# Performance work log

Measured on AMD Instinct MI355X. Metric: run time of the kernel, lower is better.

Reference implementation:

```python
import jax, jax.numpy as jnp
import numpy as np

N_NODES = 100000
IN_CH = 256
HIDDEN = 256
N_EDGES = 500000


def setup_inputs() -> dict:
    key = jax.random.key(0)
    k_emb, k_ei, k_w1, k_w2 = jax.random.split(key, 4)
    embeddings = jax.random.normal(k_emb, (N_NODES, IN_CH), dtype=jnp.float32)
    edge_index = jax.random.randint(k_ei, (2, N_EDGES), 0, N_NODES, dtype=jnp.int64)
    # Linear(in*2, hidden) and Linear(hidden, 1) weights (stored input-major for x @ W)
    s1 = 1.0 / np.sqrt(2 * IN_CH)
    s2 = 1.0 / np.sqrt(HIDDEN)
    W1 = jax.random.uniform(k_w1, (2 * IN_CH, HIDDEN), dtype=jnp.float32, minval=-s1, maxval=s1)
    b1 = jnp.zeros((HIDDEN,), dtype=jnp.float32)
    W2 = jax.random.uniform(k_w2, (HIDDEN, 1), dtype=jnp.float32, minval=-s2, maxval=s2)
    b2 = jnp.zeros((1,), dtype=jnp.float32)
    return {"embeddings": embeddings, "edge_index": edge_index,
            "W1": W1, "b1": b1, "W2": W2, "b2": b2}


def reference(embeddings, edge_index, W1, b1, W2, b2):
    src, dst = edge_index[0], edge_index[1]
    # gather [E, in] twice, concat -> [E, 2*in]
    feats = jnp.concatenate([embeddings[src], embeddings[dst]], axis=-1)
    h = jax.nn.relu(feats @ W1 + b1)          # [E, hidden]
    scores = h @ W2 + b2                      # [E, 1]
    return scores.reshape(-1)
```

## Files before the change

kernel.cpp:

```cpp
#include <hip/hip_runtime.h>

#define NN   100000
#define EE   500000
#define MPAD 100096

using bf16x8 = __attribute__((ext_vector_type(8))) short;
using f32x4  = __attribute__((ext_vector_type(4))) float;
using u16x8  = __attribute__((ext_vector_type(8))) unsigned short;

__device__ __forceinline__ unsigned short f2bf(float f) {
  unsigned int x = __builtin_bit_cast(unsigned int, f);
  x += 0x7fffu + ((x >> 16) & 1u);
  return (unsigned short)(x >> 16);
}
__device__ __forceinline__ float bf2f(unsigned short u) {
  unsigned int x = ((unsigned int)u) << 16;
  return __builtin_bit_cast(float, x);
}

__global__ void wprep_kernel(const float* __restrict__ W1, unsigned short* __restrict__ WT) {
  int id = blockIdx.x * blockDim.x + threadIdx.x;
  if (id >= 512 * 32) return;
  int j  = id >> 5;
  int cg = id & 31;
  int jc = j & 255;
  int kb = (cg << 3) + ((j >= 256) ? 256 : 0);
  u16x8 v;
#pragma unroll
  for (int t = 0; t < 8; ++t)
    v[t] = f2bf(W1[(size_t)(kb + t) * 256 + jc]);
  *reinterpret_cast<u16x8*>(WT + (size_t)j * 256 + (cg << 3)) = v;
}

__global__ __launch_bounds__(512) void gemm_pq(const float* __restrict__ emb,
                                               const unsigned short* __restrict__ WT,
                                               unsigned short* __restrict__ R) {
  __shared__ unsigned short ldsA[2][128 * 32];
  __shared__ unsigned short ldsB[2][256 * 32];

  const int t    = threadIdx.x;
  const int lane = t & 63;
  const int wave = t >> 6;
  const int wrow = wave >> 2;
  const int wcol = wave & 3;
  const int m0   = (int)(blockIdx.x >> 1) * 128;
  const int n0   = (int)(blockIdx.x & 1) * 256;

  const int arow = t >> 2, ac = t & 3;
  const bool aOk = (m0 + arow) < NN;
  const float* aSrc = emb + (size_t)(m0 + arow) * 256 + (ac << 3);
  const int aW = arow * 32 + ((ac ^ ((arow >> 1) & 3)) << 3);

  const int brow = t >> 1, bh = t & 1;
  const unsigned short* bSrc = WT + (size_t)(n0 + brow) * 256 + (bh << 4);
  const int f_b = (brow >> 1) & 3;
  const int bW0 = brow * 32 + ((((bh << 1) | 0) ^ f_b) << 3);
  const int bW1 = brow * 32 + ((((bh << 1) | 1) ^ f_b) << 3);

  const int fr = lane & 15, fq = lane >> 4;
  int aoff[4], boff[4];
#pragma unroll
  for (int m = 0; m < 4; ++m) {
    int r = wrow * 64 + 16 * m + fr;
    aoff[m] = r * 32 + ((fq ^ ((r >> 1) & 3)) << 3);
  }
#pragma unroll
  for (int n = 0; n < 4; ++n) {
    int r = wcol * 64 + 16 * n + fr;
    boff[n] = r * 32 + ((fq ^ ((r >> 1) & 3)) << 3);
  }

  f32x4 acc[4][4] = {};

  {
    float4 a0, a1;
    if (aOk) { a0 = *(const float4*)aSrc; a1 = *(const float4*)(aSrc + 4); }
    else     { a0 = make_float4(0.f, 0.f, 0.f, 0.f); a1 = a0; }
    u16x8 b0 = *(const u16x8*)bSrc;
    u16x8 b1 = *(const u16x8*)(bSrc + 8);
    u16x8 aw;
    aw[0] = f2bf(a0.x); aw[1] = f2bf(a0.y); aw[2] = f2bf(a0.z); aw[3] = f2bf(a0.w);
    aw[4] = f2bf(a1.x); aw[5] = f2bf(a1.y); aw[6] = f2bf(a1.z); aw[7] = f2bf(a1.w);
    *(u16x8*)&ldsA[0][aW]  = aw;
    *(u16x8*)&ldsB[0][bW0] = b0;
    *(u16x8*)&ldsB[0][bW1] = b1;
  }
  __syncthreads();

#pragma unroll
  for (int ks = 0; ks < 8; ++ks) {
    const int p = ks & 1;
    float4 na0, na1; u16x8 nb0, nb1;
    if (ks < 7) {
      const float* as = aSrc + ((ks + 1) << 5);
      if (aOk) { na0 = *(const float4*)as; na1 = *(const float4*)(as + 4); }
      else     { na0 = make_float4(0.f, 0.f, 0.f, 0.f); na1 = na0; }
      const unsigned short* bs = bSrc + ((ks + 1) << 5);
      nb0 = *(const u16x8*)bs;
      nb1 = *(const u16x8*)(bs + 8);
    }
    bf16x8 av[4], bv[4];
#pragma unroll
    for (int m = 0; m < 4; ++m) av[m] = *(const bf16x8*)&ldsA[p][aoff[m]];
#pragma unroll
    for (int n = 0; n < 4; ++n) bv[n] = *(const bf16x8*)&ldsB[p][boff[n]];
#pragma unroll
    for (int m = 0; m < 4; ++m)
#pragma unroll
      for (int n = 0; n < 4; ++n)
        acc[m][n] = __builtin_amdgcn_mfma_f32_16x16x32_bf16(av[m], bv[n], acc[m][n], 0, 0, 0);
    if (ks < 7) {
      u16x8 aw;
      aw[0] = f2bf(na0.x); aw[1] = f2bf(na0.y); aw[2] = f2bf(na0.z); aw[3] = f2bf(na0.w);
      aw[4] = f2bf(na1.x); aw[5] = f2bf(na1.y); aw[6] = f2bf(na1.z); aw[7] = f2bf(na1.w);
      *(u16x8*)&ldsA[p ^ 1][aW]  = aw;
      *(u16x8*)&ldsB[p ^ 1][bW0] = nb0;
      *(u16x8*)&ldsB[p ^ 1][bW1] = nb1;
    }
    __syncthreads();
  }

#pragma unroll
  for (int m = 0; m < 4; ++m) {
    const int r0 = m0 + wrow * 64 + 16 * m + (fq << 2);
#pragma unroll
    for (int n = 0; n < 4; ++n) {
      const int c = n0 + wcol * 64 + 16 * n + fr;
#pragma unroll
      for (int i = 0; i < 4; ++i)
        R[(size_t)(r0 + i) * 512 + c] = f2bf(acc[m][n][i]);
    }
  }
}

__global__ __launch_bounds__(256) void edge_kernel(const int* __restrict__ idx,
                                                   const unsigned short* __restrict__ R,
                                                   const float* __restrict__ b1,
                                                   const float* __restrict__ W2,
                                                   const float* __restrict__ b2,
                                                   float* __restrict__ out) {
  const int lane  = threadIdx.x & 63;
  const int gwave = (int)((blockIdx.x * blockDim.x + threadIdx.x) >> 6);
  const int nwave = (int)((gridDim.x * blockDim.x) >> 6);
  const float4 b1v = *(const float4*)(b1 + (lane << 2));
  const float4 w2v = *(const float4*)(W2 + (lane << 2));
  const float bias = b2[0];
  for (int e = gwave; e < EE; e += nwave) {
    const int s = idx[e];
    const int d = idx[EE + e];
    const ushort4 pa = *(const ushort4*)(R + (size_t)s * 512 + (lane << 2));
    const ushort4 pb = *(const ushort4*)(R + (size_t)d * 512 + 256 + (lane << 2));
    float acc;
    acc  = fmaxf(bf2f(pa.x) + bf2f(pb.x) + b1v.x, 0.f) * w2v.x;
    acc += fmaxf(bf2f(pa.y) + bf2f(pb.y) + b1v.y, 0.f) * w2v.y;
    acc += fmaxf(bf2f(pa.z) + bf2f(pb.z) + b1v.z, 0.f) * w2v.z;
    acc += fmaxf(bf2f(pa.w) + bf2f(pb.w) + b1v.w, 0.f) * w2v.w;
#pragma unroll
    for (int off = 32; off > 0; off >>= 1) acc += __shfl_xor(acc, off, 64);
    if (lane == 0) out[e] = acc + bias;
  }
}

__global__ __launch_bounds__(256) void fallback_kernel(const float* __restrict__ emb,
                                                       const int* __restrict__ idx,
                                                       const float* __restrict__ W1,
                                                       const float* __restrict__ b1,
                                                       const float* __restrict__ W2,
                                                       const float* __restrict__ b2,
                                                       float* __restrict__ out) {
  __shared__ float feats[512];
  __shared__ float red[256];
  const int t = threadIdx.x;
  for (int e = blockIdx.x; e < EE; e += gridDim.x) {
    __syncthreads();
    const int s = idx[e], d = idx[EE + e];
    feats[t]       = emb[(size_t)s * 256 + t];
    feats[256 + t] = emb[(size_t)d * 256 + t];
    __syncthreads();
    float h = b1[t];
    for (int k = 0; k < 512; ++k) h += feats[k] * W1[k * 256 + t];
    red[t] = fmaxf(h, 0.f) * W2[t];
    __syncthreads();
    for (int off = 128; off > 0; off >>= 1) {
      if (t < off) red[t] += red[t + off];
      __syncthreads();
    }
    if (t == 0) out[e] = red[0] + b2[0];
  }
}

extern "C" void kernel_launch(void* const* d_in, const int* in_sizes, int n_in,
                              void* d_out, int out_size, void* d_ws, size_t ws_size,
                              hipStream_t stream) {
  const float* emb = (const float*)d_in[0];
  const int*   idx = (const int*)d_in[1];
  const float* W1  = (const float*)d_in[2];
  const float* b1  = (const float*)d_in[3];
  const float* W2  = (const float*)d_in[4];
  const float* b2  = (const float*)d_in[5];
  float* out = (float*)d_out;

  const size_t wt_elems = (size_t)512 * 256;
  const size_t r_elems  = (size_t)MPAD * 512;
  const size_t need = (wt_elems + r_elems) * sizeof(unsigned short);

  if (ws_size < need) {
    fallback_kernel<<<4096, 256, 0, stream>>>(emb, idx, W1, b1, W2, b2, out);
    return;
  }

  unsigned short* WT = (unsigned short*)d_ws;
  unsigned short* R  = WT + wt_elems;

  wprep_kernel<<<64, 256, 0, stream>>>(W1, WT);
  gemm_pq<<<782 * 2, 512, 0, stream>>>(emb, WT, R);
  edge_kernel<<<2048, 256, 0, stream>>>(idx, R, b1, W2, b2, out);
}
```

Measured before the change: 160.1 us.

## Fold b1 into GEMM epilogue and gather 8 edges per wave with 16-byte loads

The b1 bias is now added in the node-GEMM epilogue, applied only to the source half of R, so the edge kernel no longer loads or adds it. The edge kernel splits each wave into two 32-lane halves and processes 8 edges per wave iteration. Each lane issues four 16-byte gathers per side, which puts more independent memory requests in flight and shortens the shuffle reduction to 5 steps. Rounding changes slightly because the bias is added before the bf16 conversion.

Measured after the change: 167.5 us. +4.7%, slower.

```diff
diff --git a/kernel.cpp b/kernel.cpp
--- a/kernel.cpp
+++ b/kernel.cpp
@@ -34,6 +34,7 @@
 
 __global__ __launch_bounds__(512) void gemm_pq(const float* __restrict__ emb,
                                                const unsigned short* __restrict__ WT,
+                                               const float* __restrict__ b1,
                                                unsigned short* __restrict__ R) {
   __shared__ unsigned short ldsA[2][128 * 32];
   __shared__ unsigned short ldsB[2][256 * 32];
@@ -77,13 +78,13 @@
     if (aOk) { a0 = *(const float4*)aSrc; a1 = *(const float4*)(aSrc + 4); }
     else     { a0 = make_float4(0.f, 0.f, 0.f, 0.f); a1 = a0; }
     u16x8 b0 = *(const u16x8*)bSrc;
-    u16x8 b1 = *(const u16x8*)(bSrc + 8);
+    u16x8 b1v = *(const u16x8*)(bSrc + 8);
     u16x8 aw;
     aw[0] = f2bf(a0.x); aw[1] = f2bf(a0.y); aw[2] = f2bf(a0.z); aw[3] = f2bf(a0.w);
     aw[4] = f2bf(a1.x); aw[5] = f2bf(a1.y); aw[6] = f2bf(a1.z); aw[7] = f2bf(a1.w);
     *(u16x8*)&ldsA[0][aW]  = aw;
     *(u16x8*)&ldsB[0][bW0] = b0;
-    *(u16x8*)&ldsB[0][bW1] = b1;
+    *(u16x8*)&ldsB[0][bW1] = b1v;
   }
   __syncthreads();
 
@@ -121,43 +122,62 @@
   }
 
 #pragma unroll
-  for (int m = 0; m < 4; ++m) {
-    const int r0 = m0 + wrow * 64 + 16 * m + (fq << 2);
-#pragma unroll
-    for (int n = 0; n < 4; ++n) {
-      const int c = n0 + wcol * 64 + 16 * n + fr;
+  for (int n = 0; n < 4; ++n) {
+    const int c = n0 + wcol * 64 + 16 * n + fr;
+    const float bn = (c < 256) ? b1[c] : 0.f;
+#pragma unroll
+    for (int m = 0; m < 4; ++m) {
+      const int r0 = m0 + wrow * 64 + 16 * m + (fq << 2);
 #pragma unroll
       for (int i = 0; i < 4; ++i)
-        R[(size_t)(r0 + i) * 512 + c] = f2bf(acc[m][n][i]);
+        R[(size_t)(r0 + i) * 512 + c] = f2bf(acc[m][n][i] + bn);
     }
   }
 }
 
 __global__ __launch_bounds__(256) void edge_kernel(const int* __restrict__ idx,
                                                    const unsigned short* __restrict__ R,
-                                                   const float* __restrict__ b1,
                                                    const float* __restrict__ W2,
                                                    const float* __restrict__ b2,
                                                    float* __restrict__ out) {
   const int lane  = threadIdx.x & 63;
+  const int half  = lane >> 5;
+  const int l     = lane & 31;
   const int gwave = (int)((blockIdx.x * blockDim.x + threadIdx.x) >> 6);
   const int nwave = (int)((gridDim.x * blockDim.x) >> 6);
-  const float4 b1v = *(const float4*)(b1 + (lane << 2));
-  const float4 w2v = *(const float4*)(W2 + (lane << 2));
+  const float4 w0 = *(const float4*)(W2 + (l << 3));
+  const float4 w1 = *(const float4*)(W2 + (l << 3) + 4);
   const float bias = b2[0];
-  for (int e = gwave; e < EE; e += nwave) {
-    const int s = idx[e];
-    const int d = idx[EE + e];
-    const ushort4 pa = *(const ushort4*)(R + (size_t)s * 512 + (lane << 2));
-    const ushort4 pb = *(const ushort4*)(R + (size_t)d * 512 + 256 + (lane << 2));
-    float acc;
-    acc  = fmaxf(bf2f(pa.x) + bf2f(pb.x) + b1v.x, 0.f) * w2v.x;
-    acc += fmaxf(bf2f(pa.y) + bf2f(pb.y) + b1v.y, 0.f) * w2v.y;
-    acc += fmaxf(bf2f(pa.z) + bf2f(pb.z) + b1v.z, 0.f) * w2v.z;
-    acc += fmaxf(bf2f(pa.w) + bf2f(pb.w) + b1v.w, 0.f) * w2v.w;
-#pragma unroll
-    for (int off = 32; off > 0; off >>= 1) acc += __shfl_xor(acc, off, 64);
-    if (lane == 0) out[e] = acc + bias;
+
+  for (int c = gwave; c < (EE / 8); c += nwave) {
+    const int e0 = c << 3;
+    int s[4], d[4];
+#pragma unroll
+    for (int u = 0; u < 4; ++u) {
+      s[u] = idx[e0 + (u << 1) + half];
+      d[u] = idx[EE + e0 + (u << 1) + half];
+    }
+    u16x8 ga[4], gb[4];
+#pragma unroll
+    for (int u = 0; u < 4; ++u) {
+      ga[u] = *(const u16x8*)(R + (size_t)s[u] * 512 + (l << 3));
+      gb[u] = *(const u16x8*)(R + (size_t)d[u] * 512 + 256 + (l << 3));
+    }
+#pragma unroll
+    for (int u = 0; u < 4; ++u) {
+      float acc;
+      acc  = fmaxf(bf2f((unsigned short)ga[u][0]) + bf2f((unsigned short)gb[u][0]), 0.f) * w0.x;
+      acc += fmaxf(bf2f((unsigned short)ga[u][1]) + bf2f((unsigned short)gb[u][1]), 0.f) * w0.y;
+      acc += fmaxf(bf2f((unsigned short)ga[u][2]) + bf2f((unsigned short)gb[u][2]), 0.f) * w0.z;
+      acc += fmaxf(bf2f((unsigned short)ga[u][3]) + bf2f((unsigned short)gb[u][3]), 0.f) * w0.w;
+      acc += fmaxf(bf2f((unsigned short)ga[u][4]) + bf2f((unsigned short)gb[u][4]), 0.f) * w1.x;
+      acc += fmaxf(bf2f((unsigned short)ga[u][5]) + bf2f((unsigned short)gb[u][5]), 0.f) * w1.y;
+      acc += fmaxf(bf2f((unsigned short)ga[u][6]) + bf2f((unsigned short)gb[u][6]), 0.f) * w1.z;
+      acc += fmaxf(bf2f((unsigned short)ga[u][7]) + bf2f((unsigned short)gb[u][7]), 0.f) * w1.w;
+#pragma unroll
+      for (int off = 16; off > 0; off >>= 1) acc += __shfl_xor(acc, off, 64);
+      if (l == 0) out[e0 + (u << 1) + half] = acc + bias;
+    }
   }
 }
 
@@ -213,6 +233,6 @@
   unsigned short* R  = WT + wt_elems;
 
   wprep_kernel<<<64, 256, 0, stream>>>(W1, WT);
-  gemm_pq<<<782 * 2, 512, 0, stream>>>(emb, WT, R);
-  edge_kernel<<<2048, 256, 0, stream>>>(idx, R, b1, W2, b2, out);
-}
+  gemm_pq<<<782 * 2, 512, 0, stream>>>(emb, WT, b1, R);
+  edge_kernel<<<2048, 256, 0, stream>>>(idx, R, W2, b2, out);
+}
```
